# Kernel tuning notes

Hardware: AMD Instinct MI355X
Metric: run time of the kernel (lower is better)

Reference implementation:

```python
import jax, jax.numpy as jnp
import numpy as np

N = 40000       # nodes
E = 640000      # edges (avg degree 16)
F_IN = 128
F_OUT = 128
EPS = 1e-6


def setup_inputs() -> dict:
    key = jax.random.key(0)
    k1, k2, k3, k4, k5 = jax.random.split(key, 5)
    x = jax.random.normal(k1, (N, F_IN), dtype=jnp.float32)
    row = jax.random.randint(k2, (E,), 0, N, dtype=jnp.int32)  # destination node per edge
    col = jax.random.randint(k3, (E,), 0, N, dtype=jnp.int32)  # source node per edge
    W = jax.random.normal(k4, (F_OUT, F_IN), dtype=jnp.float32) * (1.0 / np.sqrt(F_IN))
    b = jax.random.normal(k5, (F_OUT,), dtype=jnp.float32) * 0.01
    return {"x": x, "row": row, "col": col, "W": W, "b": b}


def reference(x, row, col, W, b):
    # spmm(adj, x): sum of neighbor features per destination node
    neigh_sum = jax.ops.segment_sum(x[col], row, num_segments=N)          # [N, F_IN]
    # spmm(adj, ones_like(x)): neighbor count per node (same across feature dim)
    deg = jax.ops.segment_sum(jnp.ones((row.shape[0],), x.dtype), row, num_segments=N)  # [N]
    neighbor_mean = neigh_sum / (deg[:, None] + EPS)                      # [N, F_IN]
    return neighbor_mean @ W.T + b                                        # [N, F_OUT]
```

## Files before the change

### kernel.cpp

```cpp
#include <hip/hip_runtime.h>
#include <hip/hip_fp16.h>


typedef short bf16x8 __attribute__((ext_vector_type(8)));
typedef float f32x4  __attribute__((ext_vector_type(4)));
typedef unsigned short ushort_t;

constexpr int NN = 40000;
constexpr int NE = 640000;
constexpr int CAP = 64;
constexpr int FILL_B   = 625;
constexpr int XCONV_B  = 5000;
constexpr int WSPLIT_B = 64;
constexpr float EPS = 1e-6f;

__device__ inline unsigned pack_split(float m) {
  unsigned fb = __float_as_uint(m);
  unsigned hb = (fb + 0x7fffu + ((fb >> 16) & 1u)) >> 16;
  float hf = __uint_as_float(hb << 16);
  float r = m - hf;
  unsigned rb = __float_as_uint(r);
  unsigned lb = (rb + 0x7fffu + ((rb >> 16) & 1u)) >> 16;
  return (hb << 16) | (lb & 0xffffu);
}

__global__ __launch_bounds__(256) void k_prep(const int4* __restrict__ row4,
                                              const int4* __restrict__ col4,
                                              int* __restrict__ cnt,
                                              int* __restrict__ csr,
                                              const float4* __restrict__ x4,
                                              uint2* __restrict__ xh,
                                              const float* __restrict__ W,
                                              ushort_t* __restrict__ Wh,
                                              ushort_t* __restrict__ Wl) {
  const int b = blockIdx.x;
  const int tid = threadIdx.x;
  if (b < FILL_B) {
    int i = b * 256 + tid;
    int4 r = row4[i];
    int4 c = col4[i];
    int p;
    p = atomicAdd(&cnt[r.x], 1); csr[r.x * CAP + p] = c.x;
    p = atomicAdd(&cnt[r.y], 1); csr[r.y * CAP + p] = c.y;
    p = atomicAdd(&cnt[r.z], 1); csr[r.z * CAP + p] = c.z;
    p = atomicAdd(&cnt[r.w], 1); csr[r.w * CAP + p] = c.w;
  } else if (b < FILL_B + XCONV_B) {
    int i = (b - FILL_B) * 256 + tid;
    float4 v = x4[i];
    __half2 h01 = __floats2half2_rn(v.x, v.y);
    __half2 h23 = __floats2half2_rn(v.z, v.w);
    uint2 o;
    o.x = *reinterpret_cast<unsigned*>(&h01);
    o.y = *reinterpret_cast<unsigned*>(&h23);
    xh[i] = o;
  } else {
    int i = (b - FILL_B - XCONV_B) * 256 + tid;
    float w = W[i];
    unsigned fb = __float_as_uint(w);
    unsigned hb = (fb + 0x7fffu + ((fb >> 16) & 1u)) >> 16;
    float hf = __uint_as_float(hb << 16);
    float r = w - hf;
    unsigned rb = __float_as_uint(r);
    unsigned lb = (rb + 0x7fffu + ((rb >> 16) & 1u)) >> 16;
    Wh[i] = (ushort_t)hb;
    Wl[i] = (ushort_t)lb;
  }
}

__global__ __launch_bounds__(256) void k_agg(const uint4* __restrict__ xh4,
                                             const int* __restrict__ csr,
                                             const int* __restrict__ cnt,
                                             uint4* __restrict__ outp) {
  const int wid  = threadIdx.x >> 6;
  const int lane = threadIdx.x & 63;
  const int qe   = lane >> 4;
  const int fl   = lane & 15;
  const int n = blockIdx.x * 4 + wid;
  const int d = cnt[n];
  const int* nb = csr + (size_t)n * CAP;
  float s0=0.f,s1=0.f,s2=0.f,s3=0.f,s4=0.f,s5=0.f,s6=0.f,s7=0.f;
  for (int j = 0; j < d; j += 16) {
#pragma unroll
    for (int u = 0; u < 4; ++u) {
      int jj = j + 4 * u + qe;
      if (jj < d) {
        int c = nb[jj];
        uint4 v = xh4[(size_t)c * 16 + fl];
        float2 f0 = __half22float2(*reinterpret_cast<const __half2*>(&v.x));
        float2 f1 = __half22float2(*reinterpret_cast<const __half2*>(&v.y));
        float2 f2 = __half22float2(*reinterpret_cast<const __half2*>(&v.z));
        float2 f3 = __half22float2(*reinterpret_cast<const __half2*>(&v.w));
        s0 += f0.x; s1 += f0.y; s2 += f1.x; s3 += f1.y;
        s4 += f2.x; s5 += f2.y; s6 += f3.x; s7 += f3.y;
      }
    }
  }
  s0 += __shfl_xor(s0, 16); s0 += __shfl_xor(s0, 32);
  s1 += __shfl_xor(s1, 16); s1 += __shfl_xor(s1, 32);
  s2 += __shfl_xor(s2, 16); s2 += __shfl_xor(s2, 32);
  s3 += __shfl_xor(s3, 16); s3 += __shfl_xor(s3, 32);
  s4 += __shfl_xor(s4, 16); s4 += __shfl_xor(s4, 32);
  s5 += __shfl_xor(s5, 16); s5 += __shfl_xor(s5, 32);
  s6 += __shfl_xor(s6, 16); s6 += __shfl_xor(s6, 32);
  s7 += __shfl_xor(s7, 16); s7 += __shfl_xor(s7, 32);
  if (qe == 0) {
    const float sc = 1.0f / ((float)d + EPS);
    uint4 o0, o1;
    o0.x = pack_split(s0 * sc); o0.y = pack_split(s1 * sc);
    o0.z = pack_split(s2 * sc); o0.w = pack_split(s3 * sc);
    o1.x = pack_split(s4 * sc); o1.y = pack_split(s5 * sc);
    o1.z = pack_split(s6 * sc); o1.w = pack_split(s7 * sc);
    outp[(size_t)n * 32 + fl * 2]     = o0;
    outp[(size_t)n * 32 + fl * 2 + 1] = o1;
  }
}

#define MFMA16(a, b, c) __builtin_amdgcn_mfma_f32_16x16x32_bf16((a), (b), (c), 0, 0, 0)

__global__ __launch_bounds__(256) void k_gemm(const unsigned* packed,
                                              const ushort_t* __restrict__ Wh,
                                              const ushort_t* __restrict__ Wl,
                                              const float* __restrict__ bias,
                                              float* out) {
  const int wid  = threadIdx.x >> 6;
  const int lane = threadIdx.x & 63;
  const int mt = blockIdx.x * 4 + wid;
  const int r  = lane & 15;
  const int kg = lane >> 4;
  const int arow = mt * 16 + r;
  f32x4 acc[8];
#pragma unroll
  for (int t = 0; t < 8; ++t) acc[t] = (f32x4){0.f, 0.f, 0.f, 0.f};
#pragma unroll
  for (int s = 0; s < 4; ++s) {
    const unsigned* ap = packed + (size_t)arow * 128 + s * 32 + kg * 8;
    const uint4 u0 = *(const uint4*)ap;
    const uint4 u1 = *(const uint4*)(ap + 4);
    bf16x8 Ah, Al;
    Ah[0] = (short)(u0.x >> 16); Al[0] = (short)u0.x;
    Ah[1] = (short)(u0.y >> 16); Al[1] = (short)u0.y;
    Ah[2] = (short)(u0.z >> 16); Al[2] = (short)u0.z;
    Ah[3] = (short)(u0.w >> 16); Al[3] = (short)u0.w;
    Ah[4] = (short)(u1.x >> 16); Al[4] = (short)u1.x;
    Ah[5] = (short)(u1.y >> 16); Al[5] = (short)u1.y;
    Ah[6] = (short)(u1.z >> 16); Al[6] = (short)u1.z;
    Ah[7] = (short)(u1.w >> 16); Al[7] = (short)u1.w;
#pragma unroll
    for (int t = 0; t < 8; ++t) {
      const size_t wo = (size_t)(t * 16 + r) * 128 + s * 32 + kg * 8;
      const bf16x8 Bh = *(const bf16x8*)(Wh + wo);
      const bf16x8 Bl = *(const bf16x8*)(Wl + wo);
      acc[t] = MFMA16(Ah, Bh, acc[t]);
      acc[t] = MFMA16(Ah, Bl, acc[t]);
      acc[t] = MFMA16(Al, Bh, acc[t]);
    }
  }
#pragma unroll
  for (int t = 0; t < 8; ++t) {
    const int f = t * 16 + r;
    const float bf = bias[f];
#pragma unroll
    for (int j = 0; j < 4; ++j) {
      const int orow = mt * 16 + kg * 4 + j;
      out[(size_t)orow * 128 + f] = acc[t][j] + bf;
    }
  }
}

extern "C" void kernel_launch(void* const* d_in, const int* in_sizes, int n_in,
                              void* d_out, int out_size, void* d_ws, size_t ws_size,
                              hipStream_t stream) {
  const float* x   = (const float*)d_in[0];
  const int*   row = (const int*)d_in[1];
  const int*   col = (const int*)d_in[2];
  const float* W   = (const float*)d_in[3];
  const float* b   = (const float*)d_in[4];
  float* out = (float*)d_out;

  char* ws = (char*)d_ws;
  uint2*    xh  = (uint2*)(ws + 0);
  int*      cnt = (int*)(ws + 10240000);
  int*      csr = (int*)(ws + 10403840);
  ushort_t* Wh  = (ushort_t*)(ws + 20643840);
  ushort_t* Wl  = (ushort_t*)(ws + 20676608);

  hipMemsetAsync(cnt, 0, NN * sizeof(int), stream);
  k_prep<<<FILL_B + XCONV_B + WSPLIT_B, 256, 0, stream>>>(
      (const int4*)row, (const int4*)col, cnt, csr,
      (const float4*)x, xh, W, Wh, Wl);
  k_agg <<<NN / 4,  256, 0, stream>>>((const uint4*)xh, csr, cnt, (uint4*)out);
  k_gemm<<<NN / 64, 256, 0, stream>>>((const unsigned*)out, Wh, Wl, b, out);
}
```

Baseline: 175.3 us.

## Build CSR via two-pass bucket binning with shared-memory atomics

Replaces the per-edge global atomic CSR fill with a two-stage build. Edges are first binned into 250 row buckets using block-local shared-memory counters and one global atomic per bucket per block. A new kernel then scatters each bucket into the fixed-capacity CSR with shared atomics. The aim is to cut global atomic contention and scattered writes, at the cost of an extra kernel launch, an intermediate buffer, and fixed bucket capacity (3072) and 16-bit packing assumptions that rely on the input distribution.

```diff
diff --git a/kernel.cpp b/kernel.cpp
--- a/kernel.cpp
+++ b/kernel.cpp
@@ -9,8 +9,11 @@
 constexpr int NN = 40000;
 constexpr int NE = 640000;
 constexpr int CAP = 64;
-constexpr int FILL_B   = 625;
-constexpr int XCONV_B  = 5000;
+constexpr int NBUCK = 250;
+constexpr int NPB   = 160;
+constexpr int CAPB  = 3072;
+constexpr int BINB    = 157;
+constexpr int XCONV_B = 5000;
 constexpr int WSPLIT_B = 64;
 constexpr float EPS = 1e-6f;
 
@@ -26,8 +29,8 @@
 
 __global__ __launch_bounds__(256) void k_prep(const int4* __restrict__ row4,
                                               const int4* __restrict__ col4,
-                                              int* __restrict__ cnt,
-                                              int* __restrict__ csr,
+                                              int* __restrict__ bcur,
+                                              unsigned* __restrict__ binned,
                                               const float4* __restrict__ x4,
                                               uint2* __restrict__ xh,
                                               const float* __restrict__ W,
@@ -35,17 +38,55 @@
                                               ushort_t* __restrict__ Wl) {
   const int b = blockIdx.x;
   const int tid = threadIdx.x;
-  if (b < FILL_B) {
-    int i = b * 256 + tid;
-    int4 r = row4[i];
-    int4 c = col4[i];
-    int p;
-    p = atomicAdd(&cnt[r.x], 1); csr[r.x * CAP + p] = c.x;
-    p = atomicAdd(&cnt[r.y], 1); csr[r.y * CAP + p] = c.y;
-    p = atomicAdd(&cnt[r.z], 1); csr[r.z * CAP + p] = c.z;
-    p = atomicAdd(&cnt[r.w], 1); csr[r.w * CAP + p] = c.w;
-  } else if (b < FILL_B + XCONV_B) {
-    int i = (b - FILL_B) * 256 + tid;
+  if (b < BINB) {
+    __shared__ int lcnt[NBUCK];
+    __shared__ int lbase[NBUCK];
+    for (int i = tid; i < NBUCK; i += 256) lcnt[i] = 0;
+    __syncthreads();
+    int4 rr[4], cc[4];
+    bool val[4];
+#pragma unroll
+    for (int k = 0; k < 4; ++k) {
+      int g = b * 1024 + k * 256 + tid;
+      val[k] = (g < NE / 4);
+      if (val[k]) { rr[k] = row4[g]; cc[k] = col4[g]; }
+    }
+#pragma unroll
+    for (int k = 0; k < 4; ++k) {
+      if (val[k]) {
+        atomicAdd(&lcnt[rr[k].x / NPB], 1);
+        atomicAdd(&lcnt[rr[k].y / NPB], 1);
+        atomicAdd(&lcnt[rr[k].z / NPB], 1);
+        atomicAdd(&lcnt[rr[k].w / NPB], 1);
+      }
+    }
+    __syncthreads();
+    for (int i = tid; i < NBUCK; i += 256) {
+      int c = lcnt[i];
+      lbase[i] = c ? atomicAdd(&bcur[i], c) : 0;
+      lcnt[i] = 0;
+    }
+    __syncthreads();
+#pragma unroll
+    for (int k = 0; k < 4; ++k) {
+      if (val[k]) {
+        int r, c, bk, p;
+        r = rr[k].x; c = cc[k].x; bk = r / NPB;
+        p = lbase[bk] + atomicAdd(&lcnt[bk], 1);
+        binned[bk * CAPB + p] = ((unsigned)(r - bk * NPB) << 16) | (unsigned)c;
+        r = rr[k].y; c = cc[k].y; bk = r / NPB;
+        p = lbase[bk] + atomicAdd(&lcnt[bk], 1);
+        binned[bk * CAPB + p] = ((unsigned)(r - bk * NPB) << 16) | (unsigned)c;
+        r = rr[k].z; c = cc[k].z; bk = r / NPB;
+        p = lbase[bk] + atomicAdd(&lcnt[bk], 1);
+        binned[bk * CAPB + p] = ((unsigned)(r - bk * NPB) << 16) | (unsigned)c;
+        r = rr[k].w; c = cc[k].w; bk = r / NPB;
+        p = lbase[bk] + atomicAdd(&lcnt[bk], 1);
+        binned[bk * CAPB + p] = ((unsigned)(r - bk * NPB) << 16) | (unsigned)c;
+      }
+    }
+  } else if (b < BINB + XCONV_B) {
+    int i = (b - BINB) * 256 + tid;
     float4 v = x4[i];
     __half2 h01 = __floats2half2_rn(v.x, v.y);
     __half2 h23 = __floats2half2_rn(v.z, v.w);
@@ -54,7 +95,7 @@
     o.y = *reinterpret_cast<unsigned*>(&h23);
     xh[i] = o;
   } else {
-    int i = (b - FILL_B - XCONV_B) * 256 + tid;
+    int i = (b - BINB - XCONV_B) * 256 + tid;
     float w = W[i];
     unsigned fb = __float_as_uint(w);
     unsigned hb = (fb + 0x7fffu + ((fb >> 16) & 1u)) >> 16;
@@ -65,6 +106,28 @@
     Wh[i] = (ushort_t)hb;
     Wl[i] = (ushort_t)lb;
   }
+}
+
+__global__ __launch_bounds__(256) void k_build(const unsigned* __restrict__ binned,
+                                               const int* __restrict__ bcur,
+                                               int* __restrict__ cnt,
+                                               int* __restrict__ csr) {
+  const int bk = blockIdx.x;
+  const int tid = threadIdx.x;
+  __shared__ int lcnt[NPB];
+  for (int i = tid; i < NPB; i += 256) lcnt[i] = 0;
+  __syncthreads();
+  const int ne = bcur[bk];
+  const unsigned* src = binned + bk * CAPB;
+  for (int i = tid; i < ne; i += 256) {
+    unsigned u = src[i];
+    int lr = (int)(u >> 16);
+    int c  = (int)(u & 0xffffu);
+    int p = atomicAdd(&lcnt[lr], 1);
+    csr[(size_t)(bk * NPB + lr) * CAP + p] = c;
+  }
+  __syncthreads();
+  for (int i = tid; i < NPB; i += 256) cnt[bk * NPB + i] = lcnt[i];
 }
 
 __global__ __launch_bounds__(256) void k_agg(const uint4* __restrict__ xh4,
@@ -178,16 +241,19 @@
   float* out = (float*)d_out;
 
   char* ws = (char*)d_ws;
-  uint2*    xh  = (uint2*)(ws + 0);
-  int*      cnt = (int*)(ws + 10240000);
-  int*      csr = (int*)(ws + 10403840);
-  ushort_t* Wh  = (ushort_t*)(ws + 20643840);
-  ushort_t* Wl  = (ushort_t*)(ws + 20676608);
-
-  hipMemsetAsync(cnt, 0, NN * sizeof(int), stream);
-  k_prep<<<FILL_B + XCONV_B + WSPLIT_B, 256, 0, stream>>>(
-      (const int4*)row, (const int4*)col, cnt, csr,
+  uint2*    xh     = (uint2*)(ws + 0);
+  int*      csr    = (int*)(ws + 10240000);
+  int*      cnt    = (int*)(ws + 20480000);
+  unsigned* binned = (unsigned*)(ws + 20640000);
+  int*      bcur   = (int*)(ws + 23712000);
+  ushort_t* Wh     = (ushort_t*)(ws + 23713024);
+  ushort_t* Wl     = (ushort_t*)(ws + 23745792);
+
+  hipMemsetAsync(bcur, 0, 1024, stream);
+  k_prep <<<BINB + XCONV_B + WSPLIT_B, 256, 0, stream>>>(
+      (const int4*)row, (const int4*)col, bcur, binned,
       (const float4*)x, xh, W, Wh, Wl);
-  k_agg <<<NN / 4,  256, 0, stream>>>((const uint4*)xh, csr, cnt, (uint4*)out);
-  k_gemm<<<NN / 64, 256, 0, stream>>>((const unsigned*)out, Wh, Wl, b, out);
-}
+  k_build<<<NBUCK,   256, 0, stream>>>(binned, bcur, cnt, csr);
+  k_agg  <<<NN / 4,  256, 0, stream>>>((const uint4*)xh, csr, cnt, (uint4*)out);
+  k_gemm <<<NN / 64, 256, 0, stream>>>((const unsigned*)out, Wh, Wl, b, out);
+}
```

New measurement: 150.2 us. -14.3%, faster.
